# Kernel optimization log

Measured on AMD Instinct MI355X. Metric: run time of the kernel, lower is better.

## Reference

```python
import jax, jax.numpy as jnp
import numpy as np
from jax import lax

D_MODEL, D_INNER, D_STATE, DT_RANK, D_CONV = 512, 1024, 16, 32, 4
B, L = 4, 1024

def setup_inputs() -> dict:
    key = jax.random.key(0)
    ks = jax.random.split(key, 10)
    s = lambda k, shp, sc=0.02: jax.random.normal(k, shp, jnp.float32) * sc
    x = jax.random.normal(ks[0], (B, L, D_MODEL), jnp.float32)
    in_proj_w = s(ks[1], (2 * D_INNER, D_MODEL))
    conv_w = s(ks[2], (D_INNER, 1, D_CONV), 0.1)
    conv_b = jnp.zeros((D_INNER,), jnp.float32)
    x_proj_w = s(ks[3], (DT_RANK + 2 * D_STATE, D_INNER))
    dt_proj_w = s(ks[4], (D_INNER, DT_RANK), DT_RANK ** -0.5)
    dt_proj_b = s(ks[5], (D_INNER,), 0.1)
    # S4D-real init: A_log = log(1..d_state) per channel
    A_log = jnp.log(jnp.tile(jnp.arange(1, D_STATE + 1, dtype=jnp.float32), (D_INNER, 1)))
    D = jnp.ones((D_INNER,), jnp.float32)
    out_proj_w = s(ks[6], (D_MODEL, D_INNER))
    return dict(x=x, in_proj_w=in_proj_w, conv_w=conv_w, conv_b=conv_b,
                x_proj_w=x_proj_w, dt_proj_w=dt_proj_w, dt_proj_b=dt_proj_b,
                A_log=A_log, D=D, out_proj_w=out_proj_w)

def _mamba_fwd(x, in_proj_w, conv_w, conv_b, x_proj_w, dt_proj_w, dt_proj_b, A_log, D, out_proj_w):
    # in_proj and split into ssm branch / gate branch
    xz = jnp.einsum('bld,ed->ble', x, in_proj_w)          # [B,L,2*d_inner]
    xc, z = jnp.split(xz, 2, axis=-1)
    # depthwise causal conv1d along L (torch pads d_conv-1 both sides then slices [:L])
    xt = jnp.transpose(xc, (0, 2, 1))                      # [B,d_inner,L]
    xt = lax.conv_general_dilated(xt, conv_w, (1,), [(D_CONV - 1, 0)],
                                  feature_group_count=D_INNER,
                                  dimension_numbers=('NCH', 'OIH', 'NCH'))
    xc = jnp.transpose(xt + conv_b[None, :, None], (0, 2, 1))  # [B,L,d_inner]
    xc = jax.nn.silu(xc)
    # input-dependent SSM params
    dbc = jnp.einsum('bld,ed->ble', xc, x_proj_w)          # [B,L,dt_rank+2*d_state]
    dt, Bm, Cm = jnp.split(dbc, [DT_RANK, DT_RANK + D_STATE], axis=-1)
    delta = jax.nn.softplus(jnp.einsum('blr,dr->bld', dt, dt_proj_w) + dt_proj_b)  # [B,L,d_inner]
    A = -jnp.exp(A_log)                                    # [d_inner,d_state]
    deltaA = jnp.exp(delta[..., None] * A)                 # [B,L,d_inner,d_state]
    deltaBx = delta[..., None] * Bm[:, :, None, :] * xc[..., None]
    # parallel (associative) scan: h_t = deltaA_t * h_{t-1} + deltaBx_t
    def combine(c1, c2):
        a1, b1 = c1
        a2, b2 = c2
        return a2 * a1, a2 * b1 + b2
    _, h = lax.associative_scan(combine, (deltaA, deltaBx), axis=1)
    y = jnp.sum(h * Cm[:, :, None, :], axis=-1) + D * xc   # [B,L,d_inner]
    y = y * jax.nn.silu(z)
    return jnp.einsum('bld,ed->ble', y, out_proj_w)        # [B,L,d_model]

def reference(x, in_proj_w, conv_w, conv_b, x_proj_w, dt_proj_w, dt_proj_b, A_log, D, out_proj_w):
    return _mamba_fwd(x, in_proj_w, conv_w, conv_b, x_proj_w, dt_proj_w, dt_proj_b, A_log, D, out_proj_w)
```

## Files before the change

### kernel.cpp

```cpp
#include <hip/hip_runtime.h>
#include <cstddef>
#include <cstdint>

#define DMODEL 512
#define DINNER 1024
#define DSTATE 16
#define DTRANK 32
#define DCONV  4
#define NB     4
#define NL     1024
#define NR     (NB * NL)
#define CH     16
#define NCHUNK (NL / CH)
#define LOG2E  1.4426950408889634f
#define LN2    0.6931471805599453f

typedef __attribute__((ext_vector_type(8))) short bf16x8;
typedef __attribute__((ext_vector_type(4))) float f32x4;

__device__ __forceinline__ unsigned short f2bf(float f) {
    unsigned u = __builtin_bit_cast(unsigned, f);
    unsigned r = u + 0x7FFFu + ((u >> 16) & 1u);
    return (unsigned short)(r >> 16);
}
__device__ __forceinline__ float bf2f(unsigned short h) {
    return __builtin_bit_cast(float, (unsigned)h << 16);
}

__device__ __forceinline__ void gload_lds16(const unsigned short* g, unsigned short* lds) {
    __builtin_amdgcn_global_load_lds(
        (const __attribute__((address_space(1))) void*)g,
        (__attribute__((address_space(3))) void*)lds, 16, 0, 0);
}

__device__ __forceinline__ void pow_chain16(float q, float* dA) {
    dA[0] = q;
    dA[1] = q * q;
    dA[2] = dA[1] * q;
    dA[3] = dA[1] * dA[1];
    dA[4] = dA[3] * q;
    dA[5] = dA[3] * dA[1];
    dA[6] = dA[3] * dA[2];
    dA[7] = dA[3] * dA[3];
    dA[8] = dA[7] * q;
    dA[9] = dA[7] * dA[1];
    dA[10] = dA[7] * dA[2];
    dA[11] = dA[7] * dA[3];
    dA[12] = dA[7] * dA[4];
    dA[13] = dA[7] * dA[5];
    dA[14] = dA[7] * dA[6];
    dA[15] = dA[7] * dA[7];
}

__global__ __launch_bounds__(256) void cast_all_kernel(
    const float* __restrict__ x, const float* __restrict__ w_in,
    const float* __restrict__ w_out, const float* __restrict__ w_xp,
    unsigned short* __restrict__ xh, unsigned short* __restrict__ wih,
    unsigned short* __restrict__ woh, unsigned short* __restrict__ xpwh)
{
    int i = blockIdx.x * 256 + threadIdx.x;
    const float* src; unsigned short* dst;
    if (i < 524288)       { src = x;     dst = xh;   }
    else if (i < 786432)  { src = w_in;  dst = wih;  i -= 524288; }
    else if (i < 917504)  { src = w_out; dst = woh;  i -= 786432; }
    else if (i < 933888)  { src = w_xp;  dst = xpwh; i -= 917504; }
    else return;
    float4 v = ((const float4*)src)[i];
    ushort4 o;
    o.x = f2bf(v.x); o.y = f2bf(v.y); o.z = f2bf(v.z); o.w = f2bf(v.w);
    ((ushort4*)dst)[i] = o;
}

template<int BN, int OUTBF>
__global__ __launch_bounds__(256) void gemm_bf16_kernel(
    const unsigned short* __restrict__ A, const unsigned short* __restrict__ Bw,
    void* __restrict__ Cv, int M, int N, int K)
{
    constexpr int BK = 64;
    constexpr int NFRAG = BN / 32;
    constexpr int BINSTR = BN / 32;
    __shared__ unsigned short As[128 * BK];
    __shared__ unsigned short Bs[BN * BK];

    const int tid  = threadIdx.x;
    const int lane = tid & 63;
    const int w    = tid >> 6;
    const int wm   = w >> 1, wn = w & 1;
    const int brow = blockIdx.y * 128;
    const int bcol = blockIdx.x * BN;

    const int srcslot = (lane & 7) ^ (lane >> 3);
    const unsigned short* ag[4];
    unsigned short* al[4];
#pragma unroll
    for (int i = 0; i < 4; ++i) {
        const int r = w * 32 + i * 8 + (lane >> 3);
        ag[i] = A + (size_t)(brow + r) * K + srcslot * 8;
        al[i] = As + (w * 256 + i * 64) * 8;
    }
    const unsigned short* bg[BINSTR];
    unsigned short* bl[BINSTR];
#pragma unroll
    for (int i = 0; i < BINSTR; ++i) {
        const int r = w * 8 * BINSTR + i * 8 + (lane >> 3);
        bg[i] = Bw + (size_t)(bcol + r) * K + srcslot * 8;
        bl[i] = Bs + (w * 64 * BINSTR + i * 64) * 8;
    }

    const int fr = lane & 15;
    const int fq = lane >> 4;
    f32x4 acc[4][NFRAG] = {};

    for (int k0 = 0; k0 < K; k0 += BK) {
#pragma unroll
        for (int i = 0; i < 4; ++i) gload_lds16(ag[i] + k0, al[i]);
#pragma unroll
        for (int i = 0; i < BINSTR; ++i) gload_lds16(bg[i] + k0, bl[i]);
        __syncthreads();
#pragma unroll
        for (int ks = 0; ks < 2; ++ks) {
            bf16x8 af[4], bfr[NFRAG];
#pragma unroll
            for (int m = 0; m < 4; ++m) {
                const int r = wm * 64 + m * 16 + fr;
                const int s = (ks * 4 + fq) ^ (r & 7);
                af[m] = *(const bf16x8*)(As + r * BK + s * 8);
            }
#pragma unroll
            for (int n = 0; n < NFRAG; ++n) {
                const int r = wn * (BN / 2) + n * 16 + fr;
                const int s = (ks * 4 + fq) ^ (r & 7);
                bfr[n] = *(const bf16x8*)(Bs + r * BK + s * 8);
            }
#pragma unroll
            for (int m = 0; m < 4; ++m)
#pragma unroll
                for (int n = 0; n < NFRAG; ++n)
                    acc[m][n] = __builtin_amdgcn_mfma_f32_16x16x32_bf16(
                        af[m], bfr[n], acc[m][n], 0, 0, 0);
        }
        __syncthreads();
    }

    const int row0 = brow + wm * 64;
    const int col0 = bcol + wn * (BN / 2);
#pragma unroll
    for (int m = 0; m < 4; ++m)
#pragma unroll
        for (int n = 0; n < NFRAG; ++n)
#pragma unroll
            for (int j = 0; j < 4; ++j) {
                const size_t ci = (size_t)(row0 + m * 16 + fq * 4 + j) * N + col0 + n * 16 + fr;
                if (OUTBF) ((unsigned short*)Cv)[ci] = f2bf(acc[m][n][j]);
                else       ((float*)Cv)[ci] = acc[m][n][j];
            }
}

__global__ __launch_bounds__(256) void conv_silu_kernel(
    const unsigned short* __restrict__ xzh, const float* __restrict__ conv_w,
    const float* __restrict__ conv_b, unsigned short* __restrict__ xch)
{
    const int idx4 = blockIdx.x * 256 + threadIdx.x;
    const int e4 = idx4 & (DINNER / 4 - 1);
    const int r  = idx4 >> 8;
    const int l  = r & (NL - 1);
    const float4 cb = ((const float4*)conv_b)[e4];
    float4 w[4];
#pragma unroll
    for (int c = 0; c < 4; ++c) w[c] = ((const float4*)conv_w)[e4 * 4 + c];
    const ushort4 uz = {0, 0, 0, 0};
    const ushort4 u0 = (l >= 3) ? ((const ushort4*)(xzh + (size_t)(r - 3) * 2 * DINNER))[e4] : uz;
    const ushort4 u1 = (l >= 2) ? ((const ushort4*)(xzh + (size_t)(r - 2) * 2 * DINNER))[e4] : uz;
    const ushort4 u2 = (l >= 1) ? ((const ushort4*)(xzh + (size_t)(r - 1) * 2 * DINNER))[e4] : uz;
    const ushort4 u3 = ((const ushort4*)(xzh + (size_t)r * 2 * DINNER))[e4];
    float4 o;
    o.x = cb.x + w[0].x * bf2f(u0.x) + w[0].y * bf2f(u1.x) + w[0].z * bf2f(u2.x) + w[0].w * bf2f(u3.x);
    o.y = cb.y + w[1].x * bf2f(u0.y) + w[1].y * bf2f(u1.y) + w[1].z * bf2f(u2.y) + w[1].w * bf2f(u3.y);
    o.z = cb.z + w[2].x * bf2f(u0.z) + w[2].y * bf2f(u1.z) + w[2].z * bf2f(u2.z) + w[2].w * bf2f(u3.z);
    o.w = cb.w + w[3].x * bf2f(u0.w) + w[3].y * bf2f(u1.w) + w[3].z * bf2f(u2.w) + w[3].w * bf2f(u3.w);
    float4 s;
    s.x = o.x * __builtin_amdgcn_rcpf(1.f + __builtin_amdgcn_exp2f(-o.x * LOG2E));
    s.y = o.y * __builtin_amdgcn_rcpf(1.f + __builtin_amdgcn_exp2f(-o.y * LOG2E));
    s.z = o.z * __builtin_amdgcn_rcpf(1.f + __builtin_amdgcn_exp2f(-o.z * LOG2E));
    s.w = o.w * __builtin_amdgcn_rcpf(1.f + __builtin_amdgcn_exp2f(-o.w * LOG2E));
    ushort4 h4;
    h4.x = f2bf(s.x); h4.y = f2bf(s.y); h4.z = f2bf(s.z); h4.w = f2bf(s.w);
    ((ushort4*)xch)[idx4] = h4;
}

#define DRT 32
__global__ __launch_bounds__(256) void delta_kernel(
    const float* __restrict__ dbc, const float* __restrict__ dtw,
    const float* __restrict__ dtb, float* __restrict__ delta)
{
    __shared__ float dlds[DRT * DTRANK];
    const int t = threadIdx.x;
    const int e = blockIdx.x * 256 + t;
    const int r0 = blockIdx.y * DRT;
    for (int i = t; i < DRT * DTRANK; i += 256) {
        const int row = i >> 5, jj = i & 31;
        dlds[i] = dbc[(size_t)(r0 + row) * 64 + jj];
    }
    float4 wv[8];
    const float4* dtw4 = (const float4*)(dtw + (size_t)e * DTRANK);
#pragma unroll
    for (int q = 0; q < 8; ++q) wv[q] = dtw4[q];
    const float bias = dtb[e];
    __syncthreads();
#pragma unroll 4
    for (int row = 0; row < DRT; ++row) {
        const float4* dl4 = (const float4*)(dlds + row * DTRANK);
        float sum = bias;
#pragma unroll
        for (int q = 0; q < 8; ++q) {
            const float4 dv = dl4[q];
            const float4 w = wv[q];
            sum += dv.x * w.x + dv.y * w.y + dv.z * w.z + dv.w * w.w;
        }
        const float u = __builtin_amdgcn_exp2f(-fabsf(sum) * LOG2E);
        delta[(size_t)(r0 + row) * DINNER + e] =
            fmaxf(sum, 0.f) + __builtin_amdgcn_logf(1.f + u) * LN2;
    }
}

__global__ __launch_bounds__(256) void scanA_kernel(
    const float* __restrict__ delta, const unsigned short* __restrict__ xch,
    const float* __restrict__ dbc, const float* __restrict__ A_log,
    float* __restrict__ chunkP, float* __restrict__ chunkS)
{
    const int tid = threadIdx.x;
    const int e = blockIdx.x * 256 + tid;
    const int b = blockIdx.y, ck = blockIdx.z;
    const int rbase = b * NL + ck * CH;

    float Aes2[DSTATE];
    const float4* al4 = (const float4*)(A_log + (size_t)e * DSTATE);
#pragma unroll
    for (int q = 0; q < 4; ++q) {
        const float4 a = al4[q];
        Aes2[q * 4 + 0] = -__expf(a.x) * LOG2E;
        Aes2[q * 4 + 1] = -__expf(a.y) * LOG2E;
        Aes2[q * 4 + 2] = -__expf(a.z) * LOG2E;
        Aes2[q * 4 + 3] = -__expf(a.w) * LOG2E;
    }
    bool fast = true;
#pragma unroll
    for (int s = 1; s < DSTATE; ++s)
        fast = fast && (fabsf(Aes2[s] - (float)(s + 1) * Aes2[0]) <= 1e-4f * fabsf(Aes2[s]));

    float S[DSTATE];
#pragma unroll
    for (int s = 0; s < DSTATE; ++s) S[s] = 0.f;
    float cum = 0.f;
    const float* dp = delta + (size_t)rbase * DINNER + e;
    const unsigned short* xp = xch + (size_t)rbase * DINNER + e;
    if (fast) {
        const float a1 = Aes2[0];
        for (int l = 0; l < CH; ++l) {
            const float dl = dp[(size_t)l * DINNER];
            const float xv = bf2f(xp[(size_t)l * DINNER]);
            const float* bu = dbc + (size_t)(rbase + l) * 64 + DTRANK;
            cum += dl;
            const float common = dl * xv;
            float dA[DSTATE];
            pow_chain16(__builtin_amdgcn_exp2f(dl * a1), dA);
#pragma unroll
            for (int s = 0; s < DSTATE; ++s)
                S[s] = fmaf(dA[s], S[s], common * bu[s]);
        }
    } else {
        for (int l = 0; l < CH; ++l) {
            const float dl = dp[(size_t)l * DINNER];
            const float xv = bf2f(xp[(size_t)l * DINNER]);
            const float* bu = dbc + (size_t)(rbase + l) * 64 + DTRANK;
            cum += dl;
            const float common = dl * xv;
#pragma unroll
            for (int s = 0; s < DSTATE; ++s) {
                const float dA = __builtin_amdgcn_exp2f(dl * Aes2[s]);
                S[s] = fmaf(dA, S[s], common * bu[s]);
            }
        }
    }
    float P[DSTATE];
    if (fast) {
        pow_chain16(__builtin_amdgcn_exp2f(cum * Aes2[0]), P);
    } else {
#pragma unroll
        for (int s = 0; s < DSTATE; ++s) P[s] = __builtin_amdgcn_exp2f(cum * Aes2[s]);
    }
    const size_t oi = (((size_t)b * NCHUNK + ck) * DINNER + e) * DSTATE;
    float4* Pp = (float4*)(chunkP + oi);
    float4* Sp = (float4*)(chunkS + oi);
#pragma unroll
    for (int q = 0; q < 4; ++q) {
        float4 pv, sv;
        pv.x = P[q * 4 + 0]; pv.y = P[q * 4 + 1]; pv.z = P[q * 4 + 2]; pv.w = P[q * 4 + 3];
        sv.x = S[q * 4 + 0]; sv.y = S[q * 4 + 1]; sv.z = S[q * 4 + 2]; sv.w = S[q * 4 + 3];
        Pp[q] = pv; Sp[q] = sv;
    }
}

__global__ __launch_bounds__(256) void scanB_kernel(
    const float* __restrict__ chunkP, float* __restrict__ chunkS)
{
    const int idx = blockIdx.x * 256 + threadIdx.x;
    const int b = idx >> 14;
    const int rem = idx & (DINNER * DSTATE - 1);
    const size_t base = (size_t)b * NCHUNK * (DINNER * DSTATE) + rem;
    float h = 0.f;
#pragma unroll 8
    for (int c = 0; c < NCHUNK; ++c) {
        const size_t i = base + (size_t)c * (DINNER * DSTATE);
        const float P = chunkP[i];
        const float S = chunkS[i];
        chunkS[i] = h;
        h = fmaf(P, h, S);
    }
}

__global__ __launch_bounds__(256) void scanC_kernel(
    const unsigned short* __restrict__ xzh, const unsigned short* __restrict__ xch,
    const float* __restrict__ dbc, const float* __restrict__ A_log,
    const float* __restrict__ Dp, const float* __restrict__ hinit,
    const float* __restrict__ delta, unsigned short* __restrict__ yh)
{
    const int tid = threadIdx.x;
    const int e = blockIdx.x * 256 + tid;
    const int b = blockIdx.y, ck = blockIdx.z;
    const int rbase = b * NL + ck * CH;

    float Aes2[DSTATE];
    const float4* al4 = (const float4*)(A_log + (size_t)e * DSTATE);
#pragma unroll
    for (int q = 0; q < 4; ++q) {
        const float4 a = al4[q];
        Aes2[q * 4 + 0] = -__expf(a.x) * LOG2E;
        Aes2[q * 4 + 1] = -__expf(a.y) * LOG2E;
        Aes2[q * 4 + 2] = -__expf(a.z) * LOG2E;
        Aes2[q * 4 + 3] = -__expf(a.w) * LOG2E;
    }
    bool fast = true;
#pragma unroll
    for (int s = 1; s < DSTATE; ++s)
        fast = fast && (fabsf(Aes2[s] - (float)(s + 1) * Aes2[0]) <= 1e-4f * fabsf(Aes2[s]));

    float h[DSTATE];
    const size_t oi = (((size_t)b * NCHUNK + ck) * DINNER + e) * DSTATE;
    const float4* h4 = (const float4*)(hinit + oi);
#pragma unroll
    for (int q = 0; q < 4; ++q) {
        const float4 v = h4[q];
        h[q * 4 + 0] = v.x; h[q * 4 + 1] = v.y; h[q * 4 + 2] = v.z; h[q * 4 + 3] = v.w;
    }
    const float Dv = Dp[e];

    const float* dp = delta + (size_t)rbase * DINNER + e;
    const unsigned short* xp = xch + (size_t)rbase * DINNER + e;
    const unsigned short* zp = xzh + (size_t)rbase * (2 * DINNER) + DINNER + e;
    unsigned short* yp = yh + (size_t)rbase * DINNER + e;

    if (fast) {
        const float a1 = Aes2[0];
        for (int l = 0; l < CH; ++l) {
            const float dl = dp[(size_t)l * DINNER];
            const float xv = bf2f(xp[(size_t)l * DINNER]);
            const float zv = bf2f(zp[(size_t)l * 2 * DINNER]);
            const float* bu = dbc + (size_t)(rbase + l) * 64 + DTRANK;
            const float common = dl * xv;
            float dA[DSTATE];
            pow_chain16(__builtin_amdgcn_exp2f(dl * a1), dA);
            float y = 0.f;
#pragma unroll
            for (int s = 0; s < DSTATE; ++s) {
                h[s] = fmaf(dA[s], h[s], common * bu[s]);
                y = fmaf(h[s], bu[DSTATE + s], y);
            }
            y = fmaf(Dv, xv, y);
            const float sig = __builtin_amdgcn_rcpf(1.f + __builtin_amdgcn_exp2f(-zv * LOG2E));
            yp[(size_t)l * DINNER] = f2bf(y * (zv * sig));
        }
    } else {
        for (int l = 0; l < CH; ++l) {
            const float dl = dp[(size_t)l * DINNER];
            const float xv = bf2f(xp[(size_t)l * DINNER]);
            const float zv = bf2f(zp[(size_t)l * 2 * DINNER]);
            const float* bu = dbc + (size_t)(rbase + l) * 64 + DTRANK;
            const float common = dl * xv;
            float y = 0.f;
#pragma unroll
            for (int s = 0; s < DSTATE; ++s) {
                const float dA = __builtin_amdgcn_exp2f(dl * Aes2[s]);
                h[s] = fmaf(dA, h[s], common * bu[s]);
                y = fmaf(h[s], bu[DSTATE + s], y);
            }
            y = fmaf(Dv, xv, y);
            const float sig = __builtin_amdgcn_rcpf(1.f + __builtin_amdgcn_exp2f(-zv * LOG2E));
            yp[(size_t)l * DINNER] = f2bf(y * (zv * sig));
        }
    }
}

extern "C" void kernel_launch(void* const* d_in, const int* in_sizes, int n_in,
                              void* d_out, int out_size, void* d_ws, size_t ws_size,
                              hipStream_t stream)
{
    const float* x          = (const float*)d_in[0];
    const float* in_proj_w  = (const float*)d_in[1];
    const float* conv_w     = (const float*)d_in[2];
    const float* conv_b     = (const float*)d_in[3];
    const float* x_proj_w   = (const float*)d_in[4];
    const float* dt_proj_w  = (const float*)d_in[5];
    const float* dt_proj_b  = (const float*)d_in[6];
    const float* A_log      = (const float*)d_in[7];
    const float* Dp         = (const float*)d_in[8];
    const float* out_proj_w = (const float*)d_in[9];
    float* out = (float*)d_out;

    float* ws     = (float*)d_ws;
    float* dbc    = ws;
    float* yb     = dbc + (size_t)NR * 64;
    float* chunkS = yb + (size_t)NR * DINNER;
    float* chunkP = chunkS + (size_t)NB * NCHUNK * DINNER * DSTATE;
    unsigned short* xzh  = (unsigned short*)(chunkP + (size_t)NB * NCHUNK * DINNER * DSTATE);
    unsigned short* xch  = xzh + (size_t)NR * 2 * DINNER;
    unsigned short* yh   = xch + (size_t)NR * DINNER;
    unsigned short* xh   = yh + (size_t)NR * DINNER;
    unsigned short* wih  = xh + (size_t)NR * DMODEL;
    unsigned short* woh  = wih + (size_t)2 * DINNER * DMODEL;
    unsigned short* xpwh = woh + (size_t)DMODEL * DINNER;

    cast_all_kernel<<<(933888 + 255) / 256, 256, 0, stream>>>(
        x, in_proj_w, out_proj_w, x_proj_w, xh, wih, woh, xpwh);

    gemm_bf16_kernel<128, 1><<<dim3(2 * DINNER / 128, NR / 128), 256, 0, stream>>>(
        xh, wih, xzh, NR, 2 * DINNER, DMODEL);
    conv_silu_kernel<<<NR * DINNER / 1024, 256, 0, stream>>>(xzh, conv_w, conv_b, xch);
    gemm_bf16_kernel<64, 0><<<dim3(1, NR / 128), 256, 0, stream>>>(
        xch, xpwh, dbc, NR, 64, DINNER);
    delta_kernel<<<dim3(DINNER / 256, NR / DRT), 256, 0, stream>>>(
        dbc, dt_proj_w, dt_proj_b, yb);
    scanA_kernel<<<dim3(DINNER / 256, NB, NCHUNK), 256, 0, stream>>>(
        yb, xch, dbc, A_log, chunkP, chunkS);
    scanB_kernel<<<NB * DINNER * DSTATE / 256, 256, 0, stream>>>(chunkP, chunkS);
    scanC_kernel<<<dim3(DINNER / 256, NB, NCHUNK), 256, 0, stream>>>(
        xzh, xch, dbc, A_log, Dp, chunkS, yb, yh);
    gemm_bf16_kernel<64, 0><<<dim3(DMODEL / 64, NR / 128), 256, 0, stream>>>(
        yh, woh, out, NR, DMODEL, DINNER);
}
```

Measured before the change: 134.8 us.

## Fuse delta projection into scan kernels and double scan chunk length

Removes the separate delta kernel and its fp32 delta buffer (B*L*d_inner floats written once and read twice). The dt_proj matvec and softplus are now recomputed inside both scanA and scanC from the dbc rows. The chunk length goes from 16 to 32, which halves the number of chunks and the chunk state traffic but also halves the grid parallelism of the scan kernels. In exchange the delta arithmetic is done twice, and each thread now reads the 32-wide dt rows directly from global memory.

```diff
diff --git a/kernel.cpp b/kernel.cpp
--- a/kernel.cpp
+++ b/kernel.cpp
@@ -10,7 +10,7 @@
 #define NB     4
 #define NL     1024
 #define NR     (NB * NL)
-#define CH     16
+#define CH     32
 #define NCHUNK (NL / CH)
 #define LOG2E  1.4426950408889634f
 #define LN2    0.6931471805599453f
@@ -50,6 +50,19 @@
     dA[13] = dA[7] * dA[5];
     dA[14] = dA[7] * dA[6];
     dA[15] = dA[7] * dA[7];
+}
+
+__device__ __forceinline__ float delta_of_row(const float* rowp, const float4* wv, float bias) {
+    const float4* db4 = (const float4*)rowp;
+    float sum = bias;
+#pragma unroll
+    for (int q = 0; q < 8; ++q) {
+        const float4 dv = db4[q];
+        const float4 w = wv[q];
+        sum += dv.x * w.x + dv.y * w.y + dv.z * w.z + dv.w * w.w;
+    }
+    const float u = __builtin_amdgcn_exp2f(-fabsf(sum) * LOG2E);
+    return fmaxf(sum, 0.f) + __builtin_amdgcn_logf(1.f + u) * LN2;
 }
 
 __global__ __launch_bounds__(256) void cast_all_kernel(
@@ -188,50 +201,22 @@
     ((ushort4*)xch)[idx4] = h4;
 }
 
-#define DRT 32
-__global__ __launch_bounds__(256) void delta_kernel(
-    const float* __restrict__ dbc, const float* __restrict__ dtw,
-    const float* __restrict__ dtb, float* __restrict__ delta)
-{
-    __shared__ float dlds[DRT * DTRANK];
-    const int t = threadIdx.x;
-    const int e = blockIdx.x * 256 + t;
-    const int r0 = blockIdx.y * DRT;
-    for (int i = t; i < DRT * DTRANK; i += 256) {
-        const int row = i >> 5, jj = i & 31;
-        dlds[i] = dbc[(size_t)(r0 + row) * 64 + jj];
-    }
-    float4 wv[8];
-    const float4* dtw4 = (const float4*)(dtw + (size_t)e * DTRANK);
-#pragma unroll
-    for (int q = 0; q < 8; ++q) wv[q] = dtw4[q];
-    const float bias = dtb[e];
-    __syncthreads();
-#pragma unroll 4
-    for (int row = 0; row < DRT; ++row) {
-        const float4* dl4 = (const float4*)(dlds + row * DTRANK);
-        float sum = bias;
-#pragma unroll
-        for (int q = 0; q < 8; ++q) {
-            const float4 dv = dl4[q];
-            const float4 w = wv[q];
-            sum += dv.x * w.x + dv.y * w.y + dv.z * w.z + dv.w * w.w;
-        }
-        const float u = __builtin_amdgcn_exp2f(-fabsf(sum) * LOG2E);
-        delta[(size_t)(r0 + row) * DINNER + e] =
-            fmaxf(sum, 0.f) + __builtin_amdgcn_logf(1.f + u) * LN2;
-    }
-}
-
 __global__ __launch_bounds__(256) void scanA_kernel(
-    const float* __restrict__ delta, const unsigned short* __restrict__ xch,
-    const float* __restrict__ dbc, const float* __restrict__ A_log,
+    const unsigned short* __restrict__ xch, const float* __restrict__ dbc,
+    const float* __restrict__ dtw, const float* __restrict__ dtb,
+    const float* __restrict__ A_log,
     float* __restrict__ chunkP, float* __restrict__ chunkS)
 {
     const int tid = threadIdx.x;
     const int e = blockIdx.x * 256 + tid;
     const int b = blockIdx.y, ck = blockIdx.z;
     const int rbase = b * NL + ck * CH;
+
+    float4 wv[8];
+    const float4* dtw4 = (const float4*)(dtw + (size_t)e * DTRANK);
+#pragma unroll
+    for (int q = 0; q < 8; ++q) wv[q] = dtw4[q];
+    const float bias = dtb[e];
 
     float Aes2[DSTATE];
     const float4* al4 = (const float4*)(A_log + (size_t)e * DSTATE);
@@ -252,14 +237,14 @@
 #pragma unroll
     for (int s = 0; s < DSTATE; ++s) S[s] = 0.f;
     float cum = 0.f;
-    const float* dp = delta + (size_t)rbase * DINNER + e;
     const unsigned short* xp = xch + (size_t)rbase * DINNER + e;
     if (fast) {
         const float a1 = Aes2[0];
         for (int l = 0; l < CH; ++l) {
-            const float dl = dp[(size_t)l * DINNER];
+            const float* rowp = dbc + (size_t)(rbase + l) * 64;
+            const float dl = delta_of_row(rowp, wv, bias);
             const float xv = bf2f(xp[(size_t)l * DINNER]);
-            const float* bu = dbc + (size_t)(rbase + l) * 64 + DTRANK;
+            const float* bu = rowp + DTRANK;
             cum += dl;
             const float common = dl * xv;
             float dA[DSTATE];
@@ -270,9 +255,10 @@
         }
     } else {
         for (int l = 0; l < CH; ++l) {
-            const float dl = dp[(size_t)l * DINNER];
+            const float* rowp = dbc + (size_t)(rbase + l) * 64;
+            const float dl = delta_of_row(rowp, wv, bias);
             const float xv = bf2f(xp[(size_t)l * DINNER]);
-            const float* bu = dbc + (size_t)(rbase + l) * 64 + DTRANK;
+            const float* bu = rowp + DTRANK;
             cum += dl;
             const float common = dl * xv;
 #pragma unroll
@@ -321,14 +307,21 @@
 
 __global__ __launch_bounds__(256) void scanC_kernel(
     const unsigned short* __restrict__ xzh, const unsigned short* __restrict__ xch,
-    const float* __restrict__ dbc, const float* __restrict__ A_log,
+    const float* __restrict__ dbc, const float* __restrict__ dtw,
+    const float* __restrict__ dtb, const float* __restrict__ A_log,
     const float* __restrict__ Dp, const float* __restrict__ hinit,
-    const float* __restrict__ delta, unsigned short* __restrict__ yh)
+    unsigned short* __restrict__ yh)
 {
     const int tid = threadIdx.x;
     const int e = blockIdx.x * 256 + tid;
     const int b = blockIdx.y, ck = blockIdx.z;
     const int rbase = b * NL + ck * CH;
+
+    float4 wv[8];
+    const float4* dtw4 = (const float4*)(dtw + (size_t)e * DTRANK);
+#pragma unroll
+    for (int q = 0; q < 8; ++q) wv[q] = dtw4[q];
+    const float bias = dtb[e];
 
     float Aes2[DSTATE];
     const float4* al4 = (const float4*)(A_log + (size_t)e * DSTATE);
@@ -355,7 +348,6 @@
     }
     const float Dv = Dp[e];
 
-    const float* dp = delta + (size_t)rbase * DINNER + e;
     const unsigned short* xp = xch + (size_t)rbase * DINNER + e;
     const unsigned short* zp = xzh + (size_t)rbase * (2 * DINNER) + DINNER + e;
     unsigned short* yp = yh + (size_t)rbase * DINNER + e;
@@ -363,10 +355,11 @@
     if (fast) {
         const float a1 = Aes2[0];
         for (int l = 0; l < CH; ++l) {
-            const float dl = dp[(size_t)l * DINNER];
+            const float* rowp = dbc + (size_t)(rbase + l) * 64;
+            const float dl = delta_of_row(rowp, wv, bias);
             const float xv = bf2f(xp[(size_t)l * DINNER]);
             const float zv = bf2f(zp[(size_t)l * 2 * DINNER]);
-            const float* bu = dbc + (size_t)(rbase + l) * 64 + DTRANK;
+            const float* bu = rowp + DTRANK;
             const float common = dl * xv;
             float dA[DSTATE];
             pow_chain16(__builtin_amdgcn_exp2f(dl * a1), dA);
@@ -382,10 +375,11 @@
         }
     } else {
         for (int l = 0; l < CH; ++l) {
-            const float dl = dp[(size_t)l * DINNER];
+            const float* rowp = dbc + (size_t)(rbase + l) * 64;
+            const float dl = delta_of_row(rowp, wv, bias);
             const float xv = bf2f(xp[(size_t)l * DINNER]);
             const float zv = bf2f(zp[(size_t)l * 2 * DINNER]);
-            const float* bu = dbc + (size_t)(rbase + l) * 64 + DTRANK;
+            const float* bu = rowp + DTRANK;
             const float common = dl * xv;
             float y = 0.f;
 #pragma unroll
@@ -419,8 +413,7 @@
 
     float* ws     = (float*)d_ws;
     float* dbc    = ws;
-    float* yb     = dbc + (size_t)NR * 64;
-    float* chunkS = yb + (size_t)NR * DINNER;
+    float* chunkS = dbc + (size_t)NR * 64;
     float* chunkP = chunkS + (size_t)NB * NCHUNK * DINNER * DSTATE;
     unsigned short* xzh  = (unsigned short*)(chunkP + (size_t)NB * NCHUNK * DINNER * DSTATE);
     unsigned short* xch  = xzh + (size_t)NR * 2 * DINNER;
@@ -438,13 +431,11 @@
     conv_silu_kernel<<<NR * DINNER / 1024, 256, 0, stream>>>(xzh, conv_w, conv_b, xch);
     gemm_bf16_kernel<64, 0><<<dim3(1, NR / 128), 256, 0, stream>>>(
         xch, xpwh, dbc, NR, 64, DINNER);
-    delta_kernel<<<dim3(DINNER / 256, NR / DRT), 256, 0, stream>>>(
-        dbc, dt_proj_w, dt_proj_b, yb);
     scanA_kernel<<<dim3(DINNER / 256, NB, NCHUNK), 256, 0, stream>>>(
-        yb, xch, dbc, A_log, chunkP, chunkS);
+        xch, dbc, dt_proj_w, dt_proj_b, A_log, chunkP, chunkS);
     scanB_kernel<<<NB * DINNER * DSTATE / 256, 256, 0, stream>>>(chunkP, chunkS);
     scanC_kernel<<<dim3(DINNER / 256, NB, NCHUNK), 256, 0, stream>>>(
-        xzh, xch, dbc, A_log, Dp, chunkS, yb, yh);
+        xzh, xch, dbc, dt_proj_w, dt_proj_b, A_log, Dp, chunkS, yh);
     gemm_bf16_kernel<64, 0><<<dim3(DMODEL / 64, NR / 128), 256, 0, stream>>>(
         yh, woh, out, NR, DMODEL, DINNER);
 }
```

New measurement: 136.9 us. Within noise of the previous version (+1.5%).
